# Kernel tuning notes

Measured on AMD Instinct MI355X. Metric: run time of the kernel, lower is better.

## Reference

```python
import jax, jax.numpy as jnp
import numpy as np

B, L, H, NH = 8, 200, 128, 4
HD = H // NH  # head_size
NEG = -(2.0 ** 32) + 1.0  # padding value from the torch code


def setup_inputs() -> dict:
    key = jax.random.key(0)
    ks = jax.random.split(key, 16)
    inp = {
        "queries": jax.random.normal(ks[0], (B, L, H), jnp.float32),
        "keys": jax.random.normal(ks[1], (B, L, H), jnp.float32),
        "time_mask": jax.random.bernoulli(ks[2], 0.1, (B, L)),
        # causal mask: True above the diagonal (future positions masked)
        "attn_mask": jnp.triu(jnp.ones((L, L), jnp.bool_), k=1),
        "time_matrix_K": jax.random.normal(ks[3], (B, L, L, H), jnp.float32) * 0.02,
        "time_matrix_V": jax.random.normal(ks[4], (B, L, L, H), jnp.float32) * 0.02,
        "dis_matrix_K": jax.random.normal(ks[5], (B, L, L, H), jnp.float32) * 0.02,
        "dis_matrix_V": jax.random.normal(ks[6], (B, L, L, H), jnp.float32) * 0.02,
        "abs_pos_K": jax.random.normal(ks[7], (B, L, H), jnp.float32) * 0.02,
        "abs_pos_V": jax.random.normal(ks[8], (B, L, H), jnp.float32) * 0.02,
        # learned linear params (torch nn.Linear: y = x @ W.T + b)
        "Wq": jax.random.normal(ks[9], (H, H), jnp.float32) / np.sqrt(H),
        "bq": jnp.zeros((H,), jnp.float32),
        "Wk": jax.random.normal(ks[10], (H, H), jnp.float32) / np.sqrt(H),
        "bk": jnp.zeros((H,), jnp.float32),
        "Wv": jax.random.normal(ks[11], (H, H), jnp.float32) / np.sqrt(H),
        "bv": jnp.zeros((H,), jnp.float32),
    }
    return inp


def _split_heads(x):
    # [B, L, H] -> [NH, B, L, HD]  (matches torch.cat(torch.split(x, HD, 2), 0))
    return jnp.transpose(x.reshape(B, L, NH, HD), (2, 0, 1, 3))


def _split_heads4(x):
    # [B, L, L, H] -> [NH, B, L, L, HD]
    return jnp.transpose(x.reshape(B, L, L, NH, HD), (3, 0, 1, 2, 4))


def reference(queries, keys, time_mask, attn_mask,
              time_matrix_K, time_matrix_V, dis_matrix_K, dis_matrix_V,
              abs_pos_K, abs_pos_V, Wq, bq, Wk, bk, Wv, bv):
    Q = _split_heads(queries @ Wq.T + bq)   # [h,B,L,d]
    K = _split_heads(keys @ Wk.T + bk)
    V = _split_heads(keys @ Wv.T + bv)
    pK = _split_heads(abs_pos_K)
    pV = _split_heads(abs_pos_V)
    tK = _split_heads4(time_matrix_K)        # [h,B,L,L,d]
    tV = _split_heads4(time_matrix_V)
    dK = _split_heads4(dis_matrix_K)
    dV = _split_heads4(dis_matrix_V)

    attn = jnp.einsum('hbqd,hbkd->hbqk', Q, K)
    attn += jnp.einsum('hbqd,hbkd->hbqk', Q, pK)
    attn += jnp.einsum('hbqkd,hbqd->hbqk', tK, Q)
    attn += jnp.einsum('hbqkd,hbqd->hbqk', dK, Q)
    attn = attn / jnp.sqrt(jnp.asarray(HD, attn.dtype))

    mask = time_mask[None, :, :, None] | attn_mask[None, None, :, :]  # [1,B,L,L]
    attn = jnp.where(mask, jnp.asarray(NEG, attn.dtype), attn)
    attn = jax.nn.softmax(attn, axis=-1)  # dropout is identity (eval)

    out = jnp.einsum('hbqk,hbkd->hbqd', attn, V)
    out += jnp.einsum('hbqk,hbkd->hbqd', attn, pV)
    out += jnp.einsum('hbqk,hbqkd->hbqd', attn, tV)
    out += jnp.einsum('hbqk,hbqkd->hbqd', attn, dV)

    # [h,B,L,d] -> [B,L,H]
    return jnp.transpose(out, (1, 2, 0, 3)).reshape(B, L, H)
```

## Files before the change

kernel.cpp:

```cpp
#include <hip/hip_runtime.h>
#include <math.h>

namespace {
constexpr int B = 8, L = 200, H = 128, NH = 4;
constexpr int LP = 224;
constexpr float NEG = -4294967295.0f;
constexpr float QSCALE = 0.17677669529663687f;
}

extern "C" __global__ __launch_bounds__(256) void tama_proj(
    const float* __restrict__ queries, const float* __restrict__ keys,
    const float* __restrict__ apK, const float* __restrict__ apV,
    const float* __restrict__ Wq, const float* __restrict__ bq,
    const float* __restrict__ Wk, const float* __restrict__ bk,
    const float* __restrict__ Wv, const float* __restrict__ bv,
    float* __restrict__ Qs, float* __restrict__ KpK, float* __restrict__ VpV)
{
    const int nrb = (B * L) / 8;
    const int which = blockIdx.x / nrb;
    const int r0 = (blockIdx.x % nrb) * 8;
    const int t = threadIdx.x;

    const float* __restrict__ x    = (which == 0) ? queries : keys;
    const float* __restrict__ W    = (which == 0) ? Wq : (which == 1) ? Wk : Wv;
    const float* __restrict__ bias = (which == 0) ? bq : (which == 1) ? bk : bv;

    __shared__ float xs[8][H];
    *(float4*)(&xs[0][0] + t * 4) = *(const float4*)(x + (size_t)r0 * H + t * 4);
    __syncthreads();

    const int d  = t & (H - 1);
    const int rh = (t >> 7) * 4;
    float a0 = 0.f, a1 = 0.f, a2 = 0.f, a3 = 0.f;
    const float4* __restrict__ wrow4 = (const float4*)(W + (size_t)d * H);
    #pragma unroll 8
    for (int j4 = 0; j4 < H / 4; ++j4) {
        const float4 w = wrow4[j4];
        const int j = j4 * 4;
        a0 += xs[rh + 0][j] * w.x + xs[rh + 0][j + 1] * w.y
            + xs[rh + 0][j + 2] * w.z + xs[rh + 0][j + 3] * w.w;
        a1 += xs[rh + 1][j] * w.x + xs[rh + 1][j + 1] * w.y
            + xs[rh + 1][j + 2] * w.z + xs[rh + 1][j + 3] * w.w;
        a2 += xs[rh + 2][j] * w.x + xs[rh + 2][j + 1] * w.y
            + xs[rh + 2][j + 2] * w.z + xs[rh + 2][j + 3] * w.w;
        a3 += xs[rh + 3][j] * w.x + xs[rh + 3][j + 1] * w.y
            + xs[rh + 3][j + 2] * w.z + xs[rh + 3][j + 3] * w.w;
    }
    const float bb = bias[d];
    float o[4] = {a0 + bb, a1 + bb, a2 + bb, a3 + bb};

    if (which == 0) {
        #pragma unroll
        for (int rr = 0; rr < 4; ++rr)
            Qs[(size_t)(r0 + rh + rr) * H + d] = o[rr] * QSCALE;
    } else if (which == 1) {
        #pragma unroll
        for (int rr = 0; rr < 4; ++rr) {
            const size_t idx = (size_t)(r0 + rh + rr) * H + d;
            KpK[idx] = o[rr] + apK[idx];
        }
    } else {
        #pragma unroll
        for (int rr = 0; rr < 4; ++rr) {
            const size_t idx = (size_t)(r0 + rh + rr) * H + d;
            VpV[idx] = o[rr] + apV[idx];
        }
    }
}

struct Burst {
    float4 a0, a1, c0, c1, e0, e1;
};

__device__ __forceinline__ Burst load_burst(
    const float* __restrict__ s1, const float* __restrict__ s2,
    const float* __restrict__ s3, int k0, int krow, int c4)
{
    int r0 = k0 + krow;
    int r1 = k0 + krow + 8;
    r0 = r0 < L ? r0 : L - 1;
    r1 = r1 < L ? r1 : L - 1;
    Burst bu;
    bu.a0 = *(const float4*)(s1 + (size_t)r0 * H + c4);
    bu.a1 = *(const float4*)(s1 + (size_t)r1 * H + c4);
    bu.c0 = *(const float4*)(s2 + (size_t)r0 * H + c4);
    bu.c1 = *(const float4*)(s2 + (size_t)r1 * H + c4);
    bu.e0 = *(const float4*)(s3 + (size_t)r0 * H + c4);
    bu.e1 = *(const float4*)(s3 + (size_t)r1 * H + c4);
    return bu;
}

extern "C" __global__ __launch_bounds__(256, 2) void tama_attn(
    const float* __restrict__ Qs, const float* __restrict__ KpK,
    const float* __restrict__ VpV, const int* __restrict__ time_mask,
    const float* __restrict__ tK, const float* __restrict__ tV,
    const float* __restrict__ dK, const float* __restrict__ dV,
    float* __restrict__ out)
{
    const int bq = (int)gridDim.x - 1 - (int)blockIdx.x;
    const int b = bq / L, q = bq - b * L;
    const int t = threadIdx.x;

    __shared__ float p[NH][LP];
    __shared__ float red[8][H];

    const int c4   = (t & 31) * 4;
    const int krow = t >> 5;
    const int h    = (t & 31) >> 3;
    const int sg   = t & 7;

    const bool tmq = time_mask[b * L + q] != 0;
    const int kA = tmq ? 0 : (q + 1);
    const int kB = tmq ? L : (q + 1);

    const float4 q4 = *(const float4*)(Qs + (size_t)bq * H + c4);
    const float* __restrict__ tKb = tK + (size_t)bq * L * H;
    const float* __restrict__ dKb = dK + (size_t)bq * L * H;
    const float* __restrict__ kpb = KpK + (size_t)b * L * H;

    if (kA > 0) {
        Burst cur = load_burst(tKb, dKb, kpb, 0, krow, c4);
        for (int k0 = 0; k0 < kA; k0 += 16) {
            Burst nxt;
            if (k0 + 16 < kA)
                nxt = load_burst(tKb, dKb, kpb, k0 + 16, krow, c4);
            const int ku0 = k0 + krow;
            const int ku1 = k0 + krow + 8;
            float s0 = q4.x * (cur.a0.x + cur.c0.x + cur.e0.x)
                     + q4.y * (cur.a0.y + cur.c0.y + cur.e0.y)
                     + q4.z * (cur.a0.z + cur.c0.z + cur.e0.z)
                     + q4.w * (cur.a0.w + cur.c0.w + cur.e0.w);
            float s1 = q4.x * (cur.a1.x + cur.c1.x + cur.e1.x)
                     + q4.y * (cur.a1.y + cur.c1.y + cur.e1.y)
                     + q4.z * (cur.a1.z + cur.c1.z + cur.e1.z)
                     + q4.w * (cur.a1.w + cur.c1.w + cur.e1.w);
            s0 += __shfl_xor(s0, 1); s0 += __shfl_xor(s0, 2); s0 += __shfl_xor(s0, 4);
            s1 += __shfl_xor(s1, 1); s1 += __shfl_xor(s1, 2); s1 += __shfl_xor(s1, 4);
            if (sg == 0 && ku0 <= q) p[h][ku0] = s0;
            if (sg == 0 && ku1 <= q) p[h][ku1] = s1;
            cur = nxt;
        }
    }
    __syncthreads();

    {
        const int wv = t >> 6;
        const int lane = t & 63;
        float s0 = p[wv][lane];
        float s1 = p[wv][lane + 64];
        float s2 = p[wv][lane + 128];
        float s3 = (lane < L - 192) ? p[wv][lane + 192] : NEG;
        if (tmq || lane > q)       s0 = NEG;
        if (tmq || lane + 64 > q)  s1 = NEG;
        if (tmq || lane + 128 > q) s2 = NEG;
        if (tmq || lane + 192 > q) s3 = NEG;
        float m = fmaxf(fmaxf(s0, s1), fmaxf(s2, s3));
        #pragma unroll
        for (int off = 32; off; off >>= 1) m = fmaxf(m, __shfl_xor(m, off));
        const float e0 = __expf(s0 - m);
        const float e1 = __expf(s1 - m);
        const float e2 = __expf(s2 - m);
        const float e3 = (lane < L - 192) ? __expf(s3 - m) : 0.f;
        float sum = e0 + e1 + e2 + e3;
        #pragma unroll
        for (int off = 32; off; off >>= 1) sum += __shfl_xor(sum, off);
        const float inv = 1.0f / sum;
        p[wv][lane]       = e0 * inv;
        p[wv][lane + 64]  = e1 * inv;
        p[wv][lane + 128] = e2 * inv;
        if (lane < L - 192) p[wv][lane + 192] = e3 * inv;
        if (lane < LP - L) p[wv][L + lane] = 0.f;
    }
    __syncthreads();

    const float* __restrict__ tVb = tV + (size_t)bq * L * H;
    const float* __restrict__ dVb = dV + (size_t)bq * L * H;
    const float* __restrict__ vpb = VpV + (size_t)b * L * H;
    float ax = 0.f, ay = 0.f, az = 0.f, aw = 0.f;
    {
        Burst cur = load_burst(tVb, dVb, vpb, 0, krow, c4);
        for (int k0 = 0; k0 < kB; k0 += 16) {
            Burst nxt;
            if (k0 + 16 < kB)
                nxt = load_burst(tVb, dVb, vpb, k0 + 16, krow, c4);
            const float pk0 = p[h][k0 + krow];
            const float pk1 = p[h][k0 + krow + 8];
            ax += pk0 * (cur.a0.x + cur.c0.x + cur.e0.x)
                + pk1 * (cur.a1.x + cur.c1.x + cur.e1.x);
            ay += pk0 * (cur.a0.y + cur.c0.y + cur.e0.y)
                + pk1 * (cur.a1.y + cur.c1.y + cur.e1.y);
            az += pk0 * (cur.a0.z + cur.c0.z + cur.e0.z)
                + pk1 * (cur.a1.z + cur.c1.z + cur.e1.z);
            aw += pk0 * (cur.a0.w + cur.c0.w + cur.e0.w)
                + pk1 * (cur.a1.w + cur.c1.w + cur.e1.w);
            cur = nxt;
        }
    }
    red[krow][c4 + 0] = ax;
    red[krow][c4 + 1] = ay;
    red[krow][c4 + 2] = az;
    red[krow][c4 + 3] = aw;
    __syncthreads();
    if (t < 32) {
        float4 r = {0.f, 0.f, 0.f, 0.f};
        #pragma unroll
        for (int j = 0; j < 8; ++j) {
            r.x += red[j][t * 4 + 0];
            r.y += red[j][t * 4 + 1];
            r.z += red[j][t * 4 + 2];
            r.w += red[j][t * 4 + 3];
        }
        *(float4*)(out + (size_t)bq * H + t * 4) = r;
    }
}

extern "C" void kernel_launch(void* const* d_in, const int* in_sizes, int n_in,
                              void* d_out, int out_size, void* d_ws, size_t ws_size,
                              hipStream_t stream)
{
    const float* queries   = (const float*)d_in[0];
    const float* keys      = (const float*)d_in[1];
    const int*   time_mask = (const int*)d_in[2];
    const float* tK  = (const float*)d_in[4];
    const float* tV  = (const float*)d_in[5];
    const float* dK  = (const float*)d_in[6];
    const float* dV  = (const float*)d_in[7];
    const float* apK = (const float*)d_in[8];
    const float* apV = (const float*)d_in[9];
    const float* Wq  = (const float*)d_in[10];
    const float* bqv = (const float*)d_in[11];
    const float* Wk  = (const float*)d_in[12];
    const float* bkv = (const float*)d_in[13];
    const float* Wv  = (const float*)d_in[14];
    const float* bvv = (const float*)d_in[15];

    float* Qs  = (float*)d_ws;
    float* KpK = Qs + (size_t)B * L * H;
    float* VpV = KpK + (size_t)B * L * H;
    float* outp = (float*)d_out;

    hipLaunchKernelGGL(tama_proj, dim3(3 * (B * L) / 8), dim3(256), 0, stream,
                       queries, keys, apK, apV, Wq, bqv, Wk, bkv, Wv, bvv,
                       Qs, KpK, VpV);
    hipLaunchKernelGGL(tama_attn, dim3(B * L), dim3(256), 0, stream,
                       Qs, KpK, VpV, time_mask, tK, tV, dK, dV, outp);
}
```

Baseline: 509.7 us.

## Stream attention operands via direct global-to-LDS async loads with double buffering

Replaces the register-held prefetch bursts in the attention kernel with per-wave double-buffered LDS staging filled by global_load_lds (16-byte) instructions, using explicit vmcnt waits. Each wave now owns its own staging slots and row set, and the first V stage is issued before the softmax so its loads overlap the normalisation. Launch bounds go from 2 to 3 blocks per CU, and the reduction buffer reuses the staging memory. The aim is to cut register pressure and hide memory latency on a streaming, latency-bound kernel. The risks are the large LDS footprint (~53KB per block) and hand-placed waitcnt/barrier ordering.

```diff
diff --git a/kernel.cpp b/kernel.cpp
--- a/kernel.cpp
+++ b/kernel.cpp
@@ -4,6 +4,7 @@
 namespace {
 constexpr int B = 8, L = 200, H = 128, NH = 4;
 constexpr int LP = 224;
+constexpr int LPAD = 228;
 constexpr float NEG = -4294967295.0f;
 constexpr float QSCALE = 0.17677669529663687f;
 }
@@ -68,29 +69,32 @@
     }
 }
 
-struct Burst {
-    float4 a0, a1, c0, c1, e0, e1;
-};
-
-__device__ __forceinline__ Burst load_burst(
-    const float* __restrict__ s1, const float* __restrict__ s2,
-    const float* __restrict__ s3, int k0, int krow, int c4)
-{
-    int r0 = k0 + krow;
-    int r1 = k0 + krow + 8;
+__device__ __forceinline__ void gll16(const float* g, float* l)
+{
+    __builtin_amdgcn_global_load_lds(
+        (const __attribute__((address_space(1))) void*)g,
+        (__attribute__((address_space(3))) void*)l, 16, 0, 0);
+}
+
+__device__ __forceinline__ void issue3(
+    const float* __restrict__ sA, const float* __restrict__ sC,
+    const float* __restrict__ sE, int k0, int rb, int cg, float* dst)
+{
+    int r0 = k0 + rb;
+    int r1 = r0 + 2;
     r0 = r0 < L ? r0 : L - 1;
     r1 = r1 < L ? r1 : L - 1;
-    Burst bu;
-    bu.a0 = *(const float4*)(s1 + (size_t)r0 * H + c4);
-    bu.a1 = *(const float4*)(s1 + (size_t)r1 * H + c4);
-    bu.c0 = *(const float4*)(s2 + (size_t)r0 * H + c4);
-    bu.c1 = *(const float4*)(s2 + (size_t)r1 * H + c4);
-    bu.e0 = *(const float4*)(s3 + (size_t)r0 * H + c4);
-    bu.e1 = *(const float4*)(s3 + (size_t)r1 * H + c4);
-    return bu;
-}
-
-extern "C" __global__ __launch_bounds__(256, 2) void tama_attn(
+    const size_t o0 = (size_t)r0 * H + (cg << 2);
+    const size_t o1 = (size_t)r1 * H + (cg << 2);
+    gll16(sA + o0, dst);
+    gll16(sA + o1, dst + 256);
+    gll16(sC + o0, dst + 512);
+    gll16(sC + o1, dst + 768);
+    gll16(sE + o0, dst + 1024);
+    gll16(sE + o1, dst + 1280);
+}
+
+extern "C" __global__ __launch_bounds__(256, 3) void tama_attn(
     const float* __restrict__ Qs, const float* __restrict__ KpK,
     const float* __restrict__ VpV, const int* __restrict__ time_mask,
     const float* __restrict__ tK, const float* __restrict__ tV,
@@ -101,13 +105,17 @@
     const int b = bq / L, q = bq - b * L;
     const int t = threadIdx.x;
 
-    __shared__ float p[NH][LP];
-    __shared__ float red[8][H];
-
-    const int c4   = (t & 31) * 4;
-    const int krow = t >> 5;
-    const int h    = (t & 31) >> 3;
-    const int sg   = t & 7;
+    __shared__ float stg[2][4][3][4][128];
+    __shared__ float p[NH][LPAD];
+
+    const int lane = t & 63;
+    const int w    = t >> 6;
+    const int ri   = lane >> 5;
+    const int cg   = lane & 31;
+    const int c4   = cg << 2;
+    const int h    = cg >> 3;
+    const int sg   = lane & 7;
+    const int rb   = (w << 2) + ri;
 
     const bool tmq = time_mask[b * L + q] != 0;
     const int kA = tmq ? 0 : (q + 1);
@@ -117,39 +125,58 @@
     const float* __restrict__ tKb = tK + (size_t)bq * L * H;
     const float* __restrict__ dKb = dK + (size_t)bq * L * H;
     const float* __restrict__ kpb = KpK + (size_t)b * L * H;
-
-    if (kA > 0) {
-        Burst cur = load_burst(tKb, dKb, kpb, 0, krow, c4);
-        for (int k0 = 0; k0 < kA; k0 += 16) {
-            Burst nxt;
-            if (k0 + 16 < kA)
-                nxt = load_burst(tKb, dKb, kpb, k0 + 16, krow, c4);
-            const int ku0 = k0 + krow;
-            const int ku1 = k0 + krow + 8;
-            float s0 = q4.x * (cur.a0.x + cur.c0.x + cur.e0.x)
-                     + q4.y * (cur.a0.y + cur.c0.y + cur.e0.y)
-                     + q4.z * (cur.a0.z + cur.c0.z + cur.e0.z)
-                     + q4.w * (cur.a0.w + cur.c0.w + cur.e0.w);
-            float s1 = q4.x * (cur.a1.x + cur.c1.x + cur.e1.x)
-                     + q4.y * (cur.a1.y + cur.c1.y + cur.e1.y)
-                     + q4.z * (cur.a1.z + cur.c1.z + cur.e1.z)
-                     + q4.w * (cur.a1.w + cur.c1.w + cur.e1.w);
+    const float* __restrict__ tVb = tV + (size_t)bq * L * H;
+    const float* __restrict__ dVb = dV + (size_t)bq * L * H;
+    const float* __restrict__ vpb = VpV + (size_t)b * L * H;
+
+    float* const st0 = &stg[0][w][0][0][0];
+    float* const st1 = &stg[1][w][0][0][0];
+
+    const int nstA = (kA + 15) >> 4;
+    if (nstA > 0) {
+        issue3(tKb, dKb, kpb, 0, rb, cg, st0);
+        for (int s = 0; s < nstA; ++s) {
+            const float* rd = (s & 1) ? st1 : st0;
+            if (s + 1 < nstA) {
+                issue3(tKb, dKb, kpb, (s + 1) << 4, rb, cg,
+                       ((s + 1) & 1) ? st1 : st0);
+                asm volatile("s_waitcnt vmcnt(6)" ::: "memory");
+            } else {
+                asm volatile("s_waitcnt vmcnt(0)" ::: "memory");
+            }
+            __builtin_amdgcn_sched_barrier(0);
+            const float4 a0  = *(const float4*)(rd + ri * 128 + c4);
+            const float4 a1  = *(const float4*)(rd + (ri + 2) * 128 + c4);
+            const float4 cc0 = *(const float4*)(rd + 512 + ri * 128 + c4);
+            const float4 cc1 = *(const float4*)(rd + 512 + (ri + 2) * 128 + c4);
+            const float4 e0  = *(const float4*)(rd + 1024 + ri * 128 + c4);
+            const float4 e1  = *(const float4*)(rd + 1024 + (ri + 2) * 128 + c4);
+            float s0 = q4.x * (a0.x + cc0.x + e0.x)
+                     + q4.y * (a0.y + cc0.y + e0.y)
+                     + q4.z * (a0.z + cc0.z + e0.z)
+                     + q4.w * (a0.w + cc0.w + e0.w);
+            float s1 = q4.x * (a1.x + cc1.x + e1.x)
+                     + q4.y * (a1.y + cc1.y + e1.y)
+                     + q4.z * (a1.z + cc1.z + e1.z)
+                     + q4.w * (a1.w + cc1.w + e1.w);
             s0 += __shfl_xor(s0, 1); s0 += __shfl_xor(s0, 2); s0 += __shfl_xor(s0, 4);
             s1 += __shfl_xor(s1, 1); s1 += __shfl_xor(s1, 2); s1 += __shfl_xor(s1, 4);
-            if (sg == 0 && ku0 <= q) p[h][ku0] = s0;
-            if (sg == 0 && ku1 <= q) p[h][ku1] = s1;
-            cur = nxt;
-        }
-    }
-    __syncthreads();
+            const int ku0 = (s << 4) + rb;
+            if (sg == 0 && ku0 <= q)     p[h][ku0] = s0;
+            if (sg == 0 && ku0 + 2 <= q) p[h][ku0 + 2] = s1;
+        }
+    }
+
+    asm volatile("s_waitcnt lgkmcnt(0)" ::: "memory");
+    issue3(tVb, dVb, vpb, 0, rb, cg, st0);
+    __builtin_amdgcn_s_barrier();
+    asm volatile("" ::: "memory");
 
     {
-        const int wv = t >> 6;
-        const int lane = t & 63;
-        float s0 = p[wv][lane];
-        float s1 = p[wv][lane + 64];
-        float s2 = p[wv][lane + 128];
-        float s3 = (lane < L - 192) ? p[wv][lane + 192] : NEG;
+        float s0 = p[w][lane];
+        float s1 = p[w][lane + 64];
+        float s2 = p[w][lane + 128];
+        float s3 = (lane < L - 192) ? p[w][lane + 192] : NEG;
         if (tmq || lane > q)       s0 = NEG;
         if (tmq || lane + 64 > q)  s1 = NEG;
         if (tmq || lane + 128 > q) s2 = NEG;
@@ -165,50 +192,59 @@
         #pragma unroll
         for (int off = 32; off; off >>= 1) sum += __shfl_xor(sum, off);
         const float inv = 1.0f / sum;
-        p[wv][lane]       = e0 * inv;
-        p[wv][lane + 64]  = e1 * inv;
-        p[wv][lane + 128] = e2 * inv;
-        if (lane < L - 192) p[wv][lane + 192] = e3 * inv;
-        if (lane < LP - L) p[wv][L + lane] = 0.f;
-    }
+        p[w][lane]       = e0 * inv;
+        p[w][lane + 64]  = e1 * inv;
+        p[w][lane + 128] = e2 * inv;
+        if (lane < L - 192) p[w][lane + 192] = e3 * inv;
+        if (lane < LP - L)  p[w][L + lane] = 0.f;
+    }
+    asm volatile("s_waitcnt lgkmcnt(0)" ::: "memory");
+    __builtin_amdgcn_s_barrier();
+    asm volatile("" ::: "memory");
+
+    float ax = 0.f, ay = 0.f, az = 0.f, aw = 0.f;
+    const int nstB = (kB + 15) >> 4;
+    for (int s = 0; s < nstB; ++s) {
+        const float* rd = (s & 1) ? st1 : st0;
+        if (s + 1 < nstB) {
+            issue3(tVb, dVb, vpb, (s + 1) << 4, rb, cg,
+                   ((s + 1) & 1) ? st1 : st0);
+            asm volatile("s_waitcnt vmcnt(6)" ::: "memory");
+        } else {
+            asm volatile("s_waitcnt vmcnt(0)" ::: "memory");
+        }
+        __builtin_amdgcn_sched_barrier(0);
+        const int ku0 = (s << 4) + rb;
+        const float pk0 = p[h][ku0];
+        const float pk1 = p[h][ku0 + 2];
+        const float4 a0  = *(const float4*)(rd + ri * 128 + c4);
+        const float4 a1  = *(const float4*)(rd + (ri + 2) * 128 + c4);
+        const float4 cc0 = *(const float4*)(rd + 512 + ri * 128 + c4);
+        const float4 cc1 = *(const float4*)(rd + 512 + (ri + 2) * 128 + c4);
+        const float4 e0  = *(const float4*)(rd + 1024 + ri * 128 + c4);
+        const float4 e1  = *(const float4*)(rd + 1024 + (ri + 2) * 128 + c4);
+        ax += pk0 * (a0.x + cc0.x + e0.x) + pk1 * (a1.x + cc1.x + e1.x);
+        ay += pk0 * (a0.y + cc0.y + e0.y) + pk1 * (a1.y + cc1.y + e1.y);
+        az += pk0 * (a0.z + cc0.z + e0.z) + pk1 * (a1.z + cc1.z + e1.z);
+        aw += pk0 * (a0.w + cc0.w + e0.w) + pk1 * (a1.w + cc1.w + e1.w);
+    }
+
     __syncthreads();
-
-    const float* __restrict__ tVb = tV + (size_t)bq * L * H;
-    const float* __restrict__ dVb = dV + (size_t)bq * L * H;
-    const float* __restrict__ vpb = VpV + (size_t)b * L * H;
-    float ax = 0.f, ay = 0.f, az = 0.f, aw = 0.f;
     {
-        Burst cur = load_burst(tVb, dVb, vpb, 0, krow, c4);
-        for (int k0 = 0; k0 < kB; k0 += 16) {
-            Burst nxt;
-            if (k0 + 16 < kB)
-                nxt = load_burst(tVb, dVb, vpb, k0 + 16, krow, c4);
-            const float pk0 = p[h][k0 + krow];
-            const float pk1 = p[h][k0 + krow + 8];
-            ax += pk0 * (cur.a0.x + cur.c0.x + cur.e0.x)
-                + pk1 * (cur.a1.x + cur.c1.x + cur.e1.x);
-            ay += pk0 * (cur.a0.y + cur.c0.y + cur.e0.y)
-                + pk1 * (cur.a1.y + cur.c1.y + cur.e1.y);
-            az += pk0 * (cur.a0.z + cur.c0.z + cur.e0.z)
-                + pk1 * (cur.a1.z + cur.c1.z + cur.e1.z);
-            aw += pk0 * (cur.a0.w + cur.c0.w + cur.e0.w)
-                + pk1 * (cur.a1.w + cur.c1.w + cur.e1.w);
-            cur = nxt;
-        }
-    }
-    red[krow][c4 + 0] = ax;
-    red[krow][c4 + 1] = ay;
-    red[krow][c4 + 2] = az;
-    red[krow][c4 + 3] = aw;
+        float* red = &stg[0][0][0][0][0];
+        float* rr = red + ((w << 1) + ri) * H + c4;
+        rr[0] = ax; rr[1] = ay; rr[2] = az; rr[3] = aw;
+    }
     __syncthreads();
     if (t < 32) {
+        const float* red = &stg[0][0][0][0][0];
         float4 r = {0.f, 0.f, 0.f, 0.f};
         #pragma unroll
         for (int j = 0; j < 8; ++j) {
-            r.x += red[j][t * 4 + 0];
-            r.y += red[j][t * 4 + 1];
-            r.z += red[j][t * 4 + 2];
-            r.w += red[j][t * 4 + 3];
+            r.x += red[j * H + t * 4 + 0];
+            r.y += red[j * H + t * 4 + 1];
+            r.z += red[j * H + t * 4 + 2];
+            r.w += red[j * H + t * 4 + 3];
         }
         *(float4*)(out + (size_t)bq * H + t * 4) = r;
     }
```

New measurement: 508.0 us. About the same (-0.3%).
